# Optimization experiments

Hardware: AMD Instinct MI355X
Metric: run time of the kernel (lower is better)

The kernel has to match this reference:

```python
import jax, jax.numpy as jnp
from jax import lax
import numpy as np
import math

IMG_H, IMG_W = 592, 800  # stride-16 image for a 50x37 feature map


def _make_anchors(fx=50, fy=37, base=8, dsr=16):
    rows = []
    for x in range(fx):
        for y in range(fy):
            for size in [base, 2 * base, 4 * base]:
                rows.append([(x - size / 2) * dsr, (y - size / 2) * dsr,
                             (x + size / 2) * dsr, (y + size / 2) * dsr])
                s = math.sqrt(size ** 2 / 2)
                rows.append([(x - s) * dsr, (y - s / 2) * dsr, (x + s) * dsr, (y + s / 2) * dsr])
                rows.append([(x - s / 2) * dsr, (y - s) * dsr, (x + s / 2) * dsr, (y + s) * dsr])
    return np.array(rows, np.float32)


def setup_inputs() -> dict:
    key = jax.random.key(0)
    k = jax.random.split(key, 8)
    B, G, H, W = 32, 20, 50, 37
    feats = jax.random.normal(k[0], (B, 512, H, W), jnp.float32)
    a = _make_anchors()
    keep = (a[:, 0] >= 0) & (a[:, 1] >= 0) & (a[:, 2] <= IMG_W) & (a[:, 3] <= IMG_H)
    idxs_inside = jnp.asarray(np.nonzero(keep)[0].astype(np.int32))
    anchors = jnp.asarray(a[keep])
    # valid xyxy GT boxes inside the image
    x1 = jax.random.uniform(k[1], (B, G)) * (IMG_W - 160)
    y1 = jax.random.uniform(k[2], (B, G)) * (IMG_H - 160)
    w = 32.0 + jax.random.uniform(k[3], (B, G)) * 96.0
    h = 32.0 + jax.random.uniform(k[4], (B, G)) * 96.0
    gt_boxes = jnp.stack([x1, y1, x1 + w, y1 + h], -1)
    W3 = jax.random.normal(k[5], (512, 512, 3, 3), jnp.float32) * 0.02
    b3 = jnp.zeros((512,), jnp.float32)
    Wcls = jax.random.normal(k[6], (18, 512, 1, 1), jnp.float32) * 0.02
    bcls = jnp.zeros((18,), jnp.float32)
    Wloc = jax.random.normal(k[7], (36, 512, 1, 1), jnp.float32) * 0.02
    bloc = jnp.zeros((36,), jnp.float32)
    return {"feats": feats, "gt_boxes": gt_boxes, "anchors": anchors,
            "W3": W3, "b3": b3, "Wcls": Wcls, "bcls": bcls,
            "Wloc": Wloc, "bloc": bloc, "idxs_inside": idxs_inside}


def _conv(x, w, b, pad):
    y = lax.conv_general_dilated(x, w, (1, 1), pad,
                                 dimension_numbers=("NCHW", "OIHW", "NCHW"))
    return y + b[None, :, None, None]


def reference(feats, gt_boxes, anchors, W3, b3, Wcls, bcls, Wloc, bloc, idxs_inside):
    B = feats.shape[0]
    rpn_conv1 = jax.nn.relu(_conv(feats, W3, b3, "SAME"))
    cls_score = _conv(rpn_conv1, Wcls, bcls, "VALID")          # [B,18,H,W]
    _, C, H, Wd = cls_score.shape
    logits = cls_score.reshape(B, 2, (C * H) // 2, Wd)          # reshape(x, 2)
    prob = jax.nn.softmax(logits, axis=1)
    prob_back = prob.reshape(B, C, H, Wd)                       # reshape back to 18
    loc_pred = _conv(rpn_conv1, Wloc, bloc, "VALID")            # [B,36,H,W]

    # select inside-image anchors
    logits_sel = logits.transpose(0, 2, 3, 1).reshape(B, -1, 2)[:, idxs_inside, :]
    loc_sel = loc_pred.transpose(0, 2, 3, 1).reshape(B, -1, 4)[:, idxs_inside, :]

    # vectorized anchors x gt IoU (replaces the triple python loop)
    ix1 = jnp.maximum(anchors[None, :, None, 0], gt_boxes[:, None, :, 0])
    iy1 = jnp.maximum(anchors[None, :, None, 1], gt_boxes[:, None, :, 1])
    ix2 = jnp.minimum(anchors[None, :, None, 2], gt_boxes[:, None, :, 2])
    iy2 = jnp.minimum(anchors[None, :, None, 3], gt_boxes[:, None, :, 3])
    inter = jnp.clip(ix2 - ix1, 0) * jnp.clip(iy2 - iy1, 0)     # [B,A,G]
    area_a = (anchors[:, 2] - anchors[:, 0]) * (anchors[:, 3] - anchors[:, 1])
    area_g = (gt_boxes[..., 2] - gt_boxes[..., 0]) * (gt_boxes[..., 3] - gt_boxes[..., 1])
    iou = inter / jnp.maximum(area_a[None, :, None] + area_g[:, None, :] - inter, 1e-8)

    max_iou = iou.max(-1)                                       # [B,A]
    matched = iou.argmax(-1)                                    # [B,A] gt index per anchor
    gt_best = iou.argmax(1)                                     # [B,G] best anchor per gt
    A = anchors.shape[0]
    is_best = jnp.zeros((B, A), bool).at[jnp.arange(B)[:, None], gt_best].set(True)
    labels = (is_best | (max_iou > 0.7)).astype(jnp.int32)      # positives=1, rest 0

    logsm = jax.nn.log_softmax(logits_sel, -1)
    loss_cls = -jnp.take_along_axis(logsm, labels[..., None], -1).mean()

    tgt = jnp.take_along_axis(gt_boxes, matched[:, :, None], axis=1)  # [B,A,4]
    d = loc_sel - tgt
    sl1 = jnp.where(jnp.abs(d) < 1.0, 0.5 * d * d, jnp.abs(d) - 0.5)
    loss_loc = (sl1 * labels[..., None].astype(sl1.dtype)).sum() / 256.0

    return prob_back, loc_pred, loss_cls, loss_loc
```

## Files before the change

kernel.cpp:

```cpp
#include <hip/hip_runtime.h>
#include <stdint.h>

typedef unsigned short u16;
typedef unsigned int   u32;
typedef unsigned long long u64;

typedef __bf16 v8bf __attribute__((ext_vector_type(8)));
typedef float  v4f  __attribute__((ext_vector_type(4)));

#define NBATCH 32
#define NCH    512
#define FH     50
#define FW     37
#define PIX    1850
#define MTOT   59200
#define KTOT   4608
#define HP     52
#define WP     39
#define NG     20
#define W3N    (NCH*KTOT)
#define WCBN   (64*512)
#define BORDN  364544

#define PROB_N 1065600
#define LC_IDX 3196800
#define LL_IDX 3196801

__device__ __forceinline__ u16 f2bf(float f) {
    u32 u = __float_as_uint(f);
    u += 0x7fffu + ((u >> 16) & 1u);
    return (u16)(u >> 16);
}

__device__ __forceinline__ void gl_lds16(const u16* g, u16* l) {
    __builtin_amdgcn_global_load_lds((const __attribute__((address_space(1))) u32*)g,
                                     (__attribute__((address_space(3))) u32*)l,
                                     16, 0, 0);
}

__global__ __launch_bounds__(256) void pad_kernel(const float* __restrict__ feats,
                                                  u16* __restrict__ fpad) {
    __shared__ float t[64][65];
    const int b  = blockIdx.z;
    const int c0 = blockIdx.y * 64;
    const int p0 = blockIdx.x * 64;
    const int tid = threadIdx.x;
    {
        const int cl = tid >> 2, seg = tid & 3;
        const float* src = feats + ((size_t)b * NCH + c0 + cl) * PIX;
        const int pbase = p0 + seg * 16;
        #pragma unroll
        for (int i = 0; i < 16; i++) {
            int p = pbase + i;
            t[cl][seg * 16 + i] = (p < PIX) ? src[p] : 0.f;
        }
    }
    __syncthreads();
    {
        const int pl = tid >> 2, cs = tid & 3;
        const int p = p0 + pl;
        if (p < PIX) {
            const int h = p / FW, w = p % FW;
            size_t dst = (((size_t)b * HP + h + 1) * WP + (w + 1)) * NCH + c0 + cs * 16;
            u32 pk[8];
            #pragma unroll
            for (int i = 0; i < 8; i++) {
                u32 lo = f2bf(t[cs * 16 + 2 * i][pl]);
                u32 hi = f2bf(t[cs * 16 + 2 * i + 1][pl]);
                pk[i] = lo | (hi << 16);
            }
            *(uint4*)&fpad[dst]     = make_uint4(pk[0], pk[1], pk[2], pk[3]);
            *(uint4*)&fpad[dst + 8] = make_uint4(pk[4], pk[5], pk[6], pk[7]);
        }
    }
}

__global__ void prep_kernel(const float* __restrict__ w3, const float* __restrict__ wcls,
                            const float* __restrict__ wloc,
                            u16* __restrict__ wbt, u16* __restrict__ wcb,
                            u16* __restrict__ fpad, float* __restrict__ out) {
    int t = blockIdx.x * 256 + threadIdx.x;
    if (t < 2) out[LC_IDX + t] = 0.f;
    if (t < W3N) {
        int co = t / KTOT, k = t % KTOT;
        int dydx = k >> 9, ci = k & 511;
        wbt[t] = f2bf(w3[((size_t)co * NCH + ci) * 9 + dydx]);
    } else if (t < W3N + WCBN) {
        int t2 = t - W3N;
        int c = t2 >> 9, ci = t2 & 511;
        float v = (c < 18) ? wcls[c * 512 + ci]
                : (c < 54) ? wloc[(c - 18) * 512 + ci] : 0.f;
        wcb[t2] = f2bf(v);
    } else if (t < W3N + WCBN + BORDN) {
        int t3 = t - (W3N + WCBN);
        int c8 = t3 & 63;
        int pi = (t3 >> 6) % 178;
        int b  = (t3 >> 6) / 178;
        int h, w;
        if (pi < 39)       { h = 0;        w = pi; }
        else if (pi < 78)  { h = 51;       w = pi - 39; }
        else if (pi < 128) { h = pi - 77;  w = 0; }
        else               { h = pi - 127; w = 38; }
        size_t dst = (((size_t)b * HP + h) * WP + w) * NCH + c8 * 8;
        *(uint4*)&fpad[dst] = make_uint4(0, 0, 0, 0);
    }
}

__global__ __launch_bounds__(256) void conv3x3_mfma(const u16* __restrict__ fpad,
                                                    const u16* __restrict__ wbt,
                                                    const float* __restrict__ b3,
                                                    u16* __restrict__ conv1) {
    __shared__ __align__(16) u16 As[128][32];
    __shared__ __align__(16) u16 Bs[128][32];

    const int lid = blockIdx.x;
    const int xcd = lid & 7;
    const int n_idx = (lid >> 3) & 3;
    const int m_idx = xcd * 58 + (lid >> 5);
    if (m_idx >= 463) return;
    const int m_base = m_idx * 128;
    const int n_base = n_idx * 128;

    const int tid = threadIdx.x;
    const int wave = tid >> 6;
    const int lane = tid & 63;

    const int row   = tid >> 2;
    const int seg_g = (tid & 3) ^ ((tid >> 3) & 3);

    int rbA[2];
    #pragma unroll
    for (int r = 0; r < 2; r++) {
        int m = m_base + r * 64 + row;
        int mm = (m < MTOT) ? m : 0;
        int b = mm / PIX, p = mm % PIX;
        int y = p / FW, x = p % FW;
        rbA[r] = ((b * HP + y) * WP + x) * NCH + seg_g * 8;
    }
    int rbB[2];
    #pragma unroll
    for (int r = 0; r < 2; r++) {
        int n = n_base + r * 64 + row;
        rbB[r] = n * KTOT + seg_g * 8;
    }

    u16* const asb = &As[0][0] + wave * 512;
    u16* const bsb = &Bs[0][0] + wave * 512;

    const int wm = (wave >> 1) * 64;
    const int wn = (wave & 1) * 64;
    const int lm = lane & 15;
    const int quad = lane >> 4;
    const int ps = (quad ^ ((lm >> 1) & 3)) * 8;

    v4f acc[4][4];
    #pragma unroll
    for (int i = 0; i < 4; i++)
        #pragma unroll
        for (int j = 0; j < 4; j++)
            #pragma unroll
            for (int r = 0; r < 4; r++) acc[i][j][r] = 0.f;

    for (int k0 = 0; k0 < KTOT; k0 += 32) {
        const int dydx = k0 >> 9;
        const int ci0  = k0 & 511;
        const int offA = ((dydx / 3) * WP + (dydx % 3)) * NCH + ci0;
        #pragma unroll
        for (int r = 0; r < 2; r++)
            gl_lds16(fpad + rbA[r] + offA, asb + r * 2048);
        #pragma unroll
        for (int r = 0; r < 2; r++)
            gl_lds16(wbt + rbB[r] + k0, bsb + r * 2048);
        __syncthreads();

        v8bf af[4], bfv[4];
        #pragma unroll
        for (int i = 0; i < 4; i++)
            af[i]  = *(const v8bf*)(&As[0][0] + (wm + i * 16 + lm) * 32 + ps);
        #pragma unroll
        for (int i = 0; i < 4; i++)
            bfv[i] = *(const v8bf*)(&Bs[0][0] + (wn + i * 16 + lm) * 32 + ps);
        #pragma unroll
        for (int i = 0; i < 4; i++)
            #pragma unroll
            for (int j = 0; j < 4; j++)
                acc[i][j] = __builtin_amdgcn_mfma_f32_16x16x32_bf16(af[i], bfv[j], acc[i][j], 0, 0, 0);
        __syncthreads();
    }

    #pragma unroll
    for (int j = 0; j < 4; j++) {
        const int n = n_base + wn + j * 16 + lm;
        const float bias = b3[n];
        #pragma unroll
        for (int i = 0; i < 4; i++) {
            #pragma unroll
            for (int r = 0; r < 4; r++) {
                int m = m_base + wm + i * 16 + quad * 4 + r;
                if (m < MTOT) {
                    float v = acc[i][j][r] + bias;
                    v = v > 0.f ? v : 0.f;
                    conv1[(size_t)m * NCH + n] = f2bf(v);
                }
            }
        }
    }
}

__global__ __launch_bounds__(256) void head_mfma(const u16* __restrict__ conv1,
                                                 const u16* __restrict__ wcb,
                                                 const float* __restrict__ bcls,
                                                 const float* __restrict__ bloc,
                                                 float* __restrict__ out) {
    __shared__ __align__(16) u16 As[128][64];
    __shared__ __align__(16) u16 Bs[64][64];
    __shared__ float ct[128][66];

    const int tid = threadIdx.x;
    const int m_base = blockIdx.x * 128;
    const int wave = tid >> 6;
    const int lane = tid & 63;
    const int srow  = tid >> 3;
    const int seg_g = (tid & 7) ^ (srow & 7);

    int rbA[4];
    #pragma unroll
    for (int r = 0; r < 4; r++) {
        int m = m_base + r * 32 + srow;
        int mm = (m < MTOT) ? m : 0;
        rbA[r] = mm * NCH + seg_g * 8;
    }
    int rbB[2];
    #pragma unroll
    for (int r = 0; r < 2; r++)
        rbB[r] = (r * 32 + srow) * NCH + seg_g * 8;

    u16* const asb = &As[0][0] + wave * 512;
    u16* const bsb = &Bs[0][0] + wave * 512;

    const int wn = wave * 16;
    const int lm = lane & 15;
    const int quad = lane >> 4;
    const int x7 = lm & 7;

    v4f acc[8];
    #pragma unroll
    for (int i = 0; i < 8; i++)
        #pragma unroll
        for (int r = 0; r < 4; r++) acc[i][r] = 0.f;

    for (int k0 = 0; k0 < NCH; k0 += 64) {
        #pragma unroll
        for (int r = 0; r < 4; r++)
            gl_lds16(conv1 + rbA[r] + k0, asb + r * 2048);
        #pragma unroll
        for (int r = 0; r < 2; r++)
            gl_lds16(wcb + rbB[r] + k0, bsb + r * 2048);
        __syncthreads();

        #pragma unroll
        for (int kh = 0; kh < 2; kh++) {
            const int ps = (((kh << 2) | quad) ^ x7) * 8;
            v8bf bf = *(const v8bf*)(&Bs[0][0] + (wn + lm) * 64 + ps);
            #pragma unroll
            for (int i = 0; i < 8; i++) {
                v8bf af = *(const v8bf*)(&As[0][0] + (i * 16 + lm) * 64 + ps);
                acc[i] = __builtin_amdgcn_mfma_f32_16x16x32_bf16(af, bf, acc[i], 0, 0, 0);
            }
        }
        __syncthreads();
    }

    const int col = wn + lm;
    const float bias = (col < 18) ? bcls[col] : (col < 54) ? bloc[col - 18] : 0.f;
    #pragma unroll
    for (int i = 0; i < 8; i++)
        #pragma unroll
        for (int r = 0; r < 4; r++)
            ct[i * 16 + quad * 4 + r][col] = acc[i][r] + bias;
    __syncthreads();

    const int c = tid >> 2;
    const int pix4 = tid & 3;
    for (int px = pix4; px < 128; px += 4) {
        const int m = m_base + px;
        if (m >= MTOT) break;
        const int b = m / PIX;
        const int p = m - b * PIX;
        if (c < 9) {
            float s0 = ct[px][c], s1 = ct[px][c + 9];
            float mx = fmaxf(s0, s1);
            float e0 = __expf(s0 - mx), e1 = __expf(s1 - mx);
            float inv = 1.f / (e0 + e1);
            out[((size_t)b * 18 + c) * PIX + p]     = e0 * inv;
            out[((size_t)b * 18 + c + 9) * PIX + p] = e1 * inv;
        } else if (c >= 18 && c < 54) {
            out[(size_t)PROB_N + ((size_t)b * 36 + (c - 18)) * PIX + p] = ct[px][c];
        }
    }
}

__global__ __launch_bounds__(256) void iouloss_kernel(const float* __restrict__ anchors,
                                                      const float* __restrict__ gtb,
                                                      const int* __restrict__ idxs,
                                                      int A,
                                                      const float* __restrict__ outr,
                                                      float* __restrict__ out) {
    __shared__ float g[NG * 4];
    __shared__ u64 keys[NG];
    __shared__ int gbest[NG];
    __shared__ float red[8];
    const int b = blockIdx.y;
    const int tid = threadIdx.x;
    if (tid < NG * 4) g[tid] = gtb[b * NG * 4 + tid];
    if (tid < NG) keys[tid] = 0ull;
    __syncthreads();

    u64 lk[NG];
    #pragma unroll
    for (int gi = 0; gi < NG; gi++) lk[gi] = 0ull;
    for (int a = tid; a < A; a += 256) {
        const float ax1 = anchors[a * 4 + 0], ay1 = anchors[a * 4 + 1];
        const float ax2 = anchors[a * 4 + 2], ay2 = anchors[a * 4 + 3];
        const float areaA = (ax2 - ax1) * (ay2 - ay1);
        const u64 atag = (u64)(0xFFFFFFFFu - (u32)a);
        #pragma unroll
        for (int gi = 0; gi < NG; gi++) {
            float gx1 = g[gi*4], gy1 = g[gi*4+1], gx2 = g[gi*4+2], gy2 = g[gi*4+3];
            float iw = fmaxf(fminf(ax2, gx2) - fmaxf(ax1, gx1), 0.f);
            float ih = fmaxf(fminf(ay2, gy2) - fmaxf(ay1, gy1), 0.f);
            float inter = iw * ih;
            float areaG = (gx2 - gx1) * (gy2 - gy1);
            float iou = inter / fmaxf(areaA + areaG - inter, 1e-8f);
            u64 key = (((u64)__float_as_uint(iou)) << 32) | atag;
            if (key > lk[gi]) lk[gi] = key;
        }
    }
    #pragma unroll
    for (int gi = 0; gi < NG; gi++) {
        u64 k = lk[gi];
        #pragma unroll
        for (int off = 32; off; off >>= 1) {
            u64 o = __shfl_xor(k, off);
            k = (o > k) ? o : k;
        }
        if ((tid & 63) == 0) atomicMax(&keys[gi], k);
    }
    __syncthreads();
    if (tid < NG) gbest[tid] = (int)(0xFFFFFFFFu - (u32)(keys[tid] & 0xFFFFFFFFull));
    __syncthreads();

    float lc = 0.f, ll = 0.f;
    for (int a = tid; a < A; a += 256) {
        const float ax1 = anchors[a * 4 + 0], ay1 = anchors[a * 4 + 1];
        const float ax2 = anchors[a * 4 + 2], ay2 = anchors[a * 4 + 3];
        const float areaA = (ax2 - ax1) * (ay2 - ay1);
        float best = -1.f;
        int bg = 0;
        #pragma unroll
        for (int gi = 0; gi < NG; gi++) {
            float gx1 = g[gi*4], gy1 = g[gi*4+1], gx2 = g[gi*4+2], gy2 = g[gi*4+3];
            float iw = fmaxf(fminf(ax2, gx2) - fmaxf(ax1, gx1), 0.f);
            float ih = fmaxf(fminf(ay2, gy2) - fmaxf(ay1, gy1), 0.f);
            float inter = iw * ih;
            float areaG = (gx2 - gx1) * (gy2 - gy1);
            float iou = inter / fmaxf(areaA + areaG - inter, 1e-8f);
            if (iou > best) { best = iou; bg = gi; }
        }
        int lbl = (best > 0.7f) ? 1 : 0;
        if (!lbl) {
            #pragma unroll
            for (int gi = 0; gi < NG; gi++) lbl |= (gbest[gi] == a);
        }
        const int idx = idxs[a];
        const int cpr = idx / PIX;
        const int rem = idx % PIX;
        float p0 = outr[((size_t)b * 18 + cpr) * PIX + rem];
        float p1 = outr[((size_t)b * 18 + cpr + 9) * PIX + rem];
        lc += -logf(lbl ? p1 : p0);
        if (lbl) {
            const int hh = idx / 333;
            const int r2 = idx % 333;
            const int ww = r2 / 9;
            const int c4 = r2 % 9;
            const int pp = hh * FW + ww;
            #pragma unroll
            for (int t = 0; t < 4; t++) {
                float lv = outr[(size_t)PROB_N + ((size_t)b * 36 + c4 * 4 + t) * PIX + pp];
                float d = lv - g[bg * 4 + t];
                float ad = fabsf(d);
                ll += (ad < 1.f) ? 0.5f * d * d : ad - 0.5f;
            }
        }
    }
    #pragma unroll
    for (int off = 32; off; off >>= 1) {
        lc += __shfl_xor(lc, off);
        ll += __shfl_xor(ll, off);
    }
    const int lane = tid & 63, wave = tid >> 6;
    if (lane == 0) { red[wave] = lc; red[4 + wave] = ll; }
    __syncthreads();
    if (tid == 0) {
        float slc = red[0] + red[1] + red[2] + red[3];
        float sll = red[4] + red[5] + red[6] + red[7];
        atomicAdd(&out[LC_IDX], slc * (1.f / (32.f * (float)A)));
        atomicAdd(&out[LL_IDX], sll * (1.f / 256.f));
    }
}

extern "C" void kernel_launch(void* const* d_in, const int* in_sizes, int n_in,
                              void* d_out, int out_size, void* d_ws, size_t ws_size,
                              hipStream_t stream) {
    const float* feats   = (const float*)d_in[0];
    const float* gtb     = (const float*)d_in[1];
    const float* anchors = (const float*)d_in[2];
    const float* W3      = (const float*)d_in[3];
    const float* b3      = (const float*)d_in[4];
    const float* Wcls    = (const float*)d_in[5];
    const float* bcls    = (const float*)d_in[6];
    const float* Wloc    = (const float*)d_in[7];
    const float* bloc    = (const float*)d_in[8];
    const int*   idxs    = (const int*)d_in[9];
    const int A = in_sizes[9];
    float* out = (float*)d_out;

    char* ws = (char*)d_ws;
    size_t off = 0;
    auto alloc = [&](size_t bytes) -> void* {
        void* p = ws + off;
        off = (off + bytes + 255) & ~(size_t)255;
        return p;
    };
    const size_t fpad_n = (size_t)NBATCH * HP * WP * NCH;
    u16* fpad   = (u16*)alloc(fpad_n * 2);
    u16* wbt    = (u16*)alloc((size_t)W3N * 2);
    u16* wcb    = (u16*)alloc((size_t)WCBN * 2);
    u16* conv1  = (u16*)alloc((size_t)MTOT * NCH * 2);

    const int prep_tot = W3N + WCBN + BORDN;
    prep_kernel<<<(prep_tot + 255) / 256, 256, 0, stream>>>(W3, Wcls, Wloc, wbt, wcb, fpad, out);
    pad_kernel<<<dim3(29, 8, NBATCH), 256, 0, stream>>>(feats, fpad);
    conv3x3_mfma<<<1856, 256, 0, stream>>>(fpad, wbt, b3, conv1);
    head_mfma<<<463, 256, 0, stream>>>(conv1, wcb, bcls, bloc, out);
    iouloss_kernel<<<dim3(1, NBATCH), 256, 0, stream>>>(anchors, gtb, idxs, A, out, out);
}
```

Before: 771.8 us.

## Rewrite conv3x3 GEMM as 256x256-tile, 8-wave double-buffered pipelined kernel

Result: no change. 778.3 us (+0.8%).

```diff
diff --git a/kernel.cpp b/kernel.cpp
--- a/kernel.cpp
+++ b/kernel.cpp
@@ -21,6 +21,7 @@
 #define W3N    (NCH*KTOT)
 #define WCBN   (64*512)
 #define BORDN  364544
+#define NT     72
 
 #define PROB_N 1065600
 #define LC_IDX 3196800
@@ -36,6 +37,12 @@
     __builtin_amdgcn_global_load_lds((const __attribute__((address_space(1))) u32*)g,
                                      (__attribute__((address_space(3))) u32*)l,
                                      16, 0, 0);
+}
+
+__device__ __forceinline__ int offA_of(int T, int kh) {
+    const int dydx = T >> 3;
+    const int ci0  = (T & 7) << 6;
+    return ((dydx / 3) * WP + (dydx % 3)) * NCH + ci0 + kh * 32;
 }
 
 __global__ __launch_bounds__(256) void pad_kernel(const float* __restrict__ feats,
@@ -106,99 +113,120 @@
     }
 }
 
-__global__ __launch_bounds__(256) void conv3x3_mfma(const u16* __restrict__ fpad,
+__global__ __launch_bounds__(512) void conv3x3_mfma(const u16* __restrict__ fpad,
                                                     const u16* __restrict__ wbt,
                                                     const float* __restrict__ b3,
                                                     u16* __restrict__ conv1) {
-    __shared__ __align__(16) u16 As[128][32];
-    __shared__ __align__(16) u16 Bs[128][32];
-
-    const int lid = blockIdx.x;
-    const int xcd = lid & 7;
-    const int n_idx = (lid >> 3) & 3;
-    const int m_idx = xcd * 58 + (lid >> 5);
-    if (m_idx >= 463) return;
-    const int m_base = m_idx * 128;
-    const int n_base = n_idx * 128;
+    __shared__ __align__(16) u16 As[2][2][256][32];
+    __shared__ __align__(16) u16 Bs[2][2][256][32];
+
+    const int wg     = ((int)blockIdx.x & 7) * 58 + ((int)blockIdx.x >> 3);
+    const int n_base = (wg & 1) * 256;
+    const int m_base = (wg >> 1) * 256;
 
     const int tid = threadIdx.x;
-    const int wave = tid >> 6;
-    const int lane = tid & 63;
-
-    const int row   = tid >> 2;
-    const int seg_g = (tid & 3) ^ ((tid >> 3) & 3);
-
-    int rbA[2];
-    #pragma unroll
-    for (int r = 0; r < 2; r++) {
-        int m = m_base + r * 64 + row;
-        int mm = (m < MTOT) ? m : 0;
-        int b = mm / PIX, p = mm % PIX;
-        int y = p / FW, x = p % FW;
-        rbA[r] = ((b * HP + y) * WP + x) * NCH + seg_g * 8;
-    }
-    int rbB[2];
-    #pragma unroll
-    for (int r = 0; r < 2; r++) {
-        int n = n_base + r * 64 + row;
-        rbB[r] = n * KTOT + seg_g * 8;
-    }
-
-    u16* const asb = &As[0][0] + wave * 512;
-    u16* const bsb = &Bs[0][0] + wave * 512;
-
-    const int wm = (wave >> 1) * 64;
-    const int wn = (wave & 1) * 64;
-    const int lm = lane & 15;
-    const int quad = lane >> 4;
-    const int ps = (quad ^ ((lm >> 1) & 3)) * 8;
-
-    v4f acc[4][4];
-    #pragma unroll
-    for (int i = 0; i < 4; i++)
+    const int w   = tid >> 6;
+    const int l   = tid & 63;
+
+    const int sr   = l >> 2;
+    const int sseg = (l & 3) ^ ((l >> 3) & 3);
+    int rbA[2], rbB[2];
+    #pragma unroll
+    for (int c = 0; c < 2; c++) {
+        const int r  = w * 32 + c * 16 + sr;
+        const int m  = m_base + r;
+        const int mm = (m < MTOT) ? m : 0;
+        const int b = mm / PIX, p = mm % PIX;
+        const int y = p / FW, x = p % FW;
+        rbA[c] = ((b * HP + y) * WP + x) * NCH + sseg * 8;
+        rbB[c] = (n_base + r) * KTOT + sseg * 8;
+    }
+    u16* const aBase = &As[0][0][0][0] + w * 1024;
+    u16* const bBase = &Bs[0][0][0][0] + w * 1024;
+
+    const int wm = w >> 2, wn = w & 3;
+    const int lm = l & 15, quad = l >> 4;
+    const int psw = (quad ^ ((lm >> 1) & 3)) * 8;
+    const u16* const aR = &As[0][0][0][0] + (wm * 128 + lm) * 32 + psw;
+    const u16* const bR = &Bs[0][0][0][0] + (wn * 64  + lm) * 32 + psw;
+
+    v4f acc[8][4];
+    #pragma unroll
+    for (int i = 0; i < 8; i++)
         #pragma unroll
         for (int j = 0; j < 4; j++)
             #pragma unroll
             for (int r = 0; r < 4; r++) acc[i][j][r] = 0.f;
 
-    for (int k0 = 0; k0 < KTOT; k0 += 32) {
-        const int dydx = k0 >> 9;
-        const int ci0  = k0 & 511;
-        const int offA = ((dydx / 3) * WP + (dydx % 3)) * NCH + ci0;
-        #pragma unroll
-        for (int r = 0; r < 2; r++)
-            gl_lds16(fpad + rbA[r] + offA, asb + r * 2048);
-        #pragma unroll
-        for (int r = 0; r < 2; r++)
-            gl_lds16(wbt + rbB[r] + k0, bsb + r * 2048);
-        __syncthreads();
-
-        v8bf af[4], bfv[4];
-        #pragma unroll
-        for (int i = 0; i < 4; i++)
-            af[i]  = *(const v8bf*)(&As[0][0] + (wm + i * 16 + lm) * 32 + ps);
-        #pragma unroll
-        for (int i = 0; i < 4; i++)
-            bfv[i] = *(const v8bf*)(&Bs[0][0] + (wn + i * 16 + lm) * 32 + ps);
-        #pragma unroll
-        for (int i = 0; i < 4; i++)
-            #pragma unroll
-            for (int j = 0; j < 4; j++)
-                acc[i][j] = __builtin_amdgcn_mfma_f32_16x16x32_bf16(af[i], bfv[j], acc[i][j], 0, 0, 0);
-        __syncthreads();
-    }
-
-    #pragma unroll
-    for (int j = 0; j < 4; j++) {
-        const int n = n_base + wn + j * 16 + lm;
+    v8bf af[4], bfv[4];
+
+#define STAGE_A(buf, kh, Tp) { \
+        const int oA_ = offA_of((Tp), (kh)); \
+        u16* const dA_ = aBase + (buf) * 16384 + (kh) * 8192; \
+        gl_lds16(fpad + rbA[0] + oA_, dA_); \
+        gl_lds16(fpad + rbA[1] + oA_, dA_ + 512); }
+#define STAGE_B(buf, kh, Tp) { \
+        const int oB_ = (Tp) * 64 + (kh) * 32; \
+        u16* const dB_ = bBase + (buf) * 16384 + (kh) * 8192; \
+        gl_lds16(wbt + rbB[0] + oB_, dB_); \
+        gl_lds16(wbt + rbB[1] + oB_, dB_ + 512); }
+
+    STAGE_A(0, 0, 0); STAGE_B(0, 0, 0);
+    STAGE_A(0, 1, 0); STAGE_B(0, 1, 0);
+    STAGE_A(1, 0, 1); STAGE_B(1, 0, 1);
+    asm volatile("s_waitcnt vmcnt(4)" ::: "memory");
+    __builtin_amdgcn_s_barrier();
+
+#define PHASE(kh, mh, STAGE_STMT, TAIL_STMT) { \
+        const int kof_ = cb * 16384 + (kh) * 8192; \
+        if ((mh) == 0) { \
+            _Pragma("unroll") \
+            for (int nj = 0; nj < 4; nj++) \
+                bfv[nj] = *(const v8bf*)(bR + kof_ + nj * 512); \
+        } \
+        _Pragma("unroll") \
+        for (int i = 0; i < 4; i++) \
+            af[i] = *(const v8bf*)(aR + kof_ + ((mh) * 4 + i) * 512); \
+        STAGE_STMT; \
+        __builtin_amdgcn_s_barrier(); \
+        asm volatile("s_waitcnt lgkmcnt(0)"); \
+        __builtin_amdgcn_sched_barrier(0); \
+        __builtin_amdgcn_s_setprio(1); \
+        _Pragma("unroll") \
+        for (int i = 0; i < 4; i++) \
+            _Pragma("unroll") \
+            for (int nj = 0; nj < 4; nj++) \
+                acc[(mh) * 4 + i][nj] = __builtin_amdgcn_mfma_f32_16x16x32_bf16( \
+                    af[i], bfv[nj], acc[(mh) * 4 + i][nj], 0, 0, 0); \
+        __builtin_amdgcn_s_setprio(0); \
+        TAIL_STMT; \
+        __builtin_amdgcn_s_barrier(); }
+
+    for (int T = 0; T < NT; ++T) {
+        const int cb = T & 1;
+        const int nb = cb ^ 1;
+        PHASE(0, 0, { if (T < NT - 1) STAGE_A(nb, 1, T + 1); }, {});
+        PHASE(0, 1, { if (T < NT - 1) STAGE_B(nb, 1, T + 1); }, {});
+        PHASE(1, 0, { if (T < NT - 2) STAGE_A(cb, 0, T + 2); }, {});
+        PHASE(1, 1, { if (T < NT - 2) STAGE_B(cb, 0, T + 2); },
+              { if (T < NT - 2)       { asm volatile("s_waitcnt vmcnt(4)" ::: "memory"); }
+                else if (T == NT - 2) { asm volatile("s_waitcnt vmcnt(0)" ::: "memory"); } });
+    }
+#undef PHASE
+#undef STAGE_A
+#undef STAGE_B
+
+    #pragma unroll
+    for (int nj = 0; nj < 4; nj++) {
+        const int n = n_base + wn * 64 + nj * 16 + lm;
         const float bias = b3[n];
         #pragma unroll
-        for (int i = 0; i < 4; i++) {
+        for (int i = 0; i < 8; i++) {
             #pragma unroll
             for (int r = 0; r < 4; r++) {
-                int m = m_base + wm + i * 16 + quad * 4 + r;
+                const int m = m_base + wm * 128 + i * 16 + quad * 4 + r;
                 if (m < MTOT) {
-                    float v = acc[i][j][r] + bias;
+                    float v = acc[i][nj][r] + bias;
                     v = v > 0.f ? v : 0.f;
                     conv1[(size_t)m * NCH + n] = f2bf(v);
                 }
@@ -441,7 +469,7 @@
     const int prep_tot = W3N + WCBN + BORDN;
     prep_kernel<<<(prep_tot + 255) / 256, 256, 0, stream>>>(W3, Wcls, Wloc, wbt, wcb, fpad, out);
     pad_kernel<<<dim3(29, 8, NBATCH), 256, 0, stream>>>(feats, fpad);
-    conv3x3_mfma<<<1856, 256, 0, stream>>>(fpad, wbt, b3, conv1);
+    conv3x3_mfma<<<464, 512, 0, stream>>>(fpad, wbt, b3, conv1);
     head_mfma<<<463, 256, 0, stream>>>(conv1, wcb, bcls, bloc, out);
     iouloss_kernel<<<dim3(1, NBATCH), 256, 0, stream>>>(anchors, gtb, idxs, A, out, out);
 }
```

## Double-buffer conv3x3 LDS tiles and retile weights into per-k-step blocks

Applied to the files above, without the earlier changes.

New measurement: 780.0 us. Within noise of the previous version (+1.1%).

```diff
diff --git a/kernel.cpp b/kernel.cpp
--- a/kernel.cpp
+++ b/kernel.cpp
@@ -21,6 +21,7 @@
 #define W3N    (NCH*KTOT)
 #define WCBN   (64*512)
 #define BORDN  364544
+#define NT32   144
 
 #define PROB_N 1065600
 #define LC_IDX 3196800
@@ -36,6 +37,12 @@
     __builtin_amdgcn_global_load_lds((const __attribute__((address_space(1))) u32*)g,
                                      (__attribute__((address_space(3))) u32*)l,
                                      16, 0, 0);
+}
+
+__device__ __forceinline__ int offA32(int T) {
+    const int dydx = T >> 4;
+    const int ci0  = (T & 15) << 5;
+    return ((dydx / 3) * WP + (dydx % 3)) * NCH + ci0;
 }
 
 __global__ __launch_bounds__(256) void pad_kernel(const float* __restrict__ feats,
@@ -82,9 +89,12 @@
     int t = blockIdx.x * 256 + threadIdx.x;
     if (t < 2) out[LC_IDX + t] = 0.f;
     if (t < W3N) {
-        int co = t / KTOT, k = t % KTOT;
+        int T = t >> 14;
+        int n = (t >> 5) & 511;
+        int c = t & 31;
+        int k = T * 32 + c;
         int dydx = k >> 9, ci = k & 511;
-        wbt[t] = f2bf(w3[((size_t)co * NCH + ci) * 9 + dydx]);
+        wbt[t] = f2bf(w3[((size_t)n * NCH + ci) * 9 + dydx]);
     } else if (t < W3N + WCBN) {
         int t2 = t - W3N;
         int c = t2 >> 9, ci = t2 & 511;
@@ -106,52 +116,46 @@
     }
 }
 
-__global__ __launch_bounds__(256) void conv3x3_mfma(const u16* __restrict__ fpad,
-                                                    const u16* __restrict__ wbt,
-                                                    const float* __restrict__ b3,
-                                                    u16* __restrict__ conv1) {
-    __shared__ __align__(16) u16 As[128][32];
-    __shared__ __align__(16) u16 Bs[128][32];
-
-    const int lid = blockIdx.x;
-    const int xcd = lid & 7;
-    const int n_idx = (lid >> 3) & 3;
-    const int m_idx = xcd * 58 + (lid >> 5);
-    if (m_idx >= 463) return;
+__global__ __launch_bounds__(256, 4) void conv3x3_mfma(const u16* __restrict__ fpad,
+                                                       const u16* __restrict__ wbt,
+                                                       const float* __restrict__ b3,
+                                                       u16* __restrict__ conv1) {
+    __shared__ __align__(16) u16 As[2][128][32];
+    __shared__ __align__(16) u16 Bs[2][128][32];
+
+    const int orig = (int)blockIdx.x;
+    const int xcd = orig & 7, idx = orig >> 3;
+    const int wg = (xcd < 4 ? xcd * 232 : 928 + (xcd - 4) * 231) + idx;
+    const int n_idx = wg / 463;
+    const int m_idx = wg - n_idx * 463;
     const int m_base = m_idx * 128;
     const int n_base = n_idx * 128;
 
     const int tid = threadIdx.x;
-    const int wave = tid >> 6;
-    const int lane = tid & 63;
-
-    const int row   = tid >> 2;
-    const int seg_g = (tid & 3) ^ ((tid >> 3) & 3);
-
-    int rbA[2];
-    #pragma unroll
-    for (int r = 0; r < 2; r++) {
-        int m = m_base + r * 64 + row;
-        int mm = (m < MTOT) ? m : 0;
-        int b = mm / PIX, p = mm % PIX;
-        int y = p / FW, x = p % FW;
-        rbA[r] = ((b * HP + y) * WP + x) * NCH + seg_g * 8;
-    }
-    int rbB[2];
-    #pragma unroll
-    for (int r = 0; r < 2; r++) {
-        int n = n_base + r * 64 + row;
-        rbB[r] = n * KTOT + seg_g * 8;
-    }
-
-    u16* const asb = &As[0][0] + wave * 512;
-    u16* const bsb = &Bs[0][0] + wave * 512;
-
-    const int wm = (wave >> 1) * 64;
-    const int wn = (wave & 1) * 64;
-    const int lm = lane & 15;
-    const int quad = lane >> 4;
+    const int w   = tid >> 6;
+    const int l   = tid & 63;
+
+    const int sr   = l >> 2;
+    const int sseg = (l & 3) ^ ((l >> 3) & 3);
+    int rbA[2], rbB[2];
+    #pragma unroll
+    for (int c = 0; c < 2; c++) {
+        const int row = w * 32 + c * 16 + sr;
+        const int m  = m_base + row;
+        const int mm = (m < MTOT) ? m : 0;
+        const int b = mm / PIX, p = mm % PIX;
+        const int y = p / FW, x = p % FW;
+        rbA[c] = ((b * HP + y) * WP + x) * NCH + sseg * 8;
+        rbB[c] = (n_base + row) * 32 + sseg * 8;
+    }
+    u16* const aBase = &As[0][0][0] + w * 1024;
+    u16* const bBase = &Bs[0][0][0] + w * 1024;
+
+    const int wm = w >> 1, wn = w & 1;
+    const int lm = l & 15, quad = l >> 4;
     const int ps = (quad ^ ((lm >> 1) & 3)) * 8;
+    const u16* const aR = &As[0][0][0] + (wm * 64 + lm) * 32 + ps;
+    const u16* const bR = &Bs[0][0][0] + (wn * 64 + lm) * 32 + ps;
 
     v4f acc[4][4];
     #pragma unroll
@@ -161,44 +165,52 @@
             #pragma unroll
             for (int r = 0; r < 4; r++) acc[i][j][r] = 0.f;
 
-    for (int k0 = 0; k0 < KTOT; k0 += 32) {
-        const int dydx = k0 >> 9;
-        const int ci0  = k0 & 511;
-        const int offA = ((dydx / 3) * WP + (dydx % 3)) * NCH + ci0;
-        #pragma unroll
-        for (int r = 0; r < 2; r++)
-            gl_lds16(fpad + rbA[r] + offA, asb + r * 2048);
-        #pragma unroll
-        for (int r = 0; r < 2; r++)
-            gl_lds16(wbt + rbB[r] + k0, bsb + r * 2048);
-        __syncthreads();
-
-        v8bf af[4], bfv[4];
+#define STAGE(buf, Tp) { \
+        const int oA_ = offA32(Tp); \
+        u16* const dA_ = aBase + (buf) * 4096; \
+        gl_lds16(fpad + rbA[0] + oA_, dA_); \
+        gl_lds16(fpad + rbA[1] + oA_, dA_ + 512); \
+        const u16* const sB_ = wbt + (size_t)(Tp) * 16384; \
+        u16* const dB_ = bBase + (buf) * 4096; \
+        gl_lds16(sB_ + rbB[0], dB_); \
+        gl_lds16(sB_ + rbB[1], dB_ + 512); }
+
+    STAGE(0, 0);
+
+    for (int T = 0; T < NT32; ++T) {
+        const int cb = T & 1;
+        const int nb = cb ^ 1;
+        asm volatile("s_waitcnt vmcnt(0)" ::: "memory");
+        __builtin_amdgcn_s_barrier();
+        if (T + 1 < NT32) STAGE(nb, T + 1);
+        v8bf av[4], bv[4];
         #pragma unroll
         for (int i = 0; i < 4; i++)
-            af[i]  = *(const v8bf*)(&As[0][0] + (wm + i * 16 + lm) * 32 + ps);
+            av[i] = *(const v8bf*)(aR + cb * 4096 + i * 512);
+        #pragma unroll
+        for (int j = 0; j < 4; j++)
+            bv[j] = *(const v8bf*)(bR + cb * 4096 + j * 512);
+        __builtin_amdgcn_s_setprio(1);
         #pragma unroll
         for (int i = 0; i < 4; i++)
-            bfv[i] = *(const v8bf*)(&Bs[0][0] + (wn + i * 16 + lm) * 32 + ps);
-        #pragma unroll
-        for (int i = 0; i < 4; i++)
             #pragma unroll
             for (int j = 0; j < 4; j++)
-                acc[i][j] = __builtin_amdgcn_mfma_f32_16x16x32_bf16(af[i], bfv[j], acc[i][j], 0, 0, 0);
-        __syncthreads();
-    }
-
-    #pragma unroll
-    for (int j = 0; j < 4; j++) {
-        const int n = n_base + wn + j * 16 + lm;
+                acc[i][j] = __builtin_amdgcn_mfma_f32_16x16x32_bf16(av[i], bv[j], acc[i][j], 0, 0, 0);
+        __builtin_amdgcn_s_setprio(0);
+    }
+#undef STAGE
+
+    #pragma unroll
+    for (int nj = 0; nj < 4; nj++) {
+        const int n = n_base + wn * 64 + nj * 16 + lm;
         const float bias = b3[n];
         #pragma unroll
         for (int i = 0; i < 4; i++) {
             #pragma unroll
             for (int r = 0; r < 4; r++) {
-                int m = m_base + wm + i * 16 + quad * 4 + r;
+                const int m = m_base + wm * 64 + i * 16 + quad * 4 + r;
                 if (m < MTOT) {
-                    float v = acc[i][j][r] + bias;
+                    float v = acc[i][nj][r] + bias;
                     v = v > 0.f ? v : 0.f;
                     conv1[(size_t)m * NCH + n] = f2bf(v);
                 }
@@ -441,7 +453,7 @@
     const int prep_tot = W3N + WCBN + BORDN;
     prep_kernel<<<(prep_tot + 255) / 256, 256, 0, stream>>>(W3, Wcls, Wloc, wbt, wcb, fpad, out);
     pad_kernel<<<dim3(29, 8, NBATCH), 256, 0, stream>>>(feats, fpad);
-    conv3x3_mfma<<<1856, 256, 0, stream>>>(fpad, wbt, b3, conv1);
+    conv3x3_mfma<<<1852, 256, 0, stream>>>(fpad, wbt, b3, conv1);
     head_mfma<<<463, 256, 0, stream>>>(conv1, wcb, bcls, bloc, out);
     iouloss_kernel<<<dim3(1, NBATCH), 256, 0, stream>>>(anchors, gtb, idxs, A, out, out);
 }
```
